# Kernel optimization log

Hardware: AMD Instinct MI355X
Metric: run time of the kernel (lower is better)

The kernel has to match this reference:

```python
import jax, jax.numpy as jnp
import numpy as np

H = W = 128
BS = 16
# Ragged per-canvas stroke counts (sum = 2048)
LENGTHS = np.array([64, 192, 128, 96, 160, 224, 32, 128, 128, 256, 64, 96, 160, 128, 96, 96], dtype=np.int64)
L = int(LENGTHS.sum())


def setup_inputs() -> dict:
    key = jax.random.key(0)
    k1, k2, k3 = jax.random.split(key, 3)
    u = jax.random.uniform(k1, (L, 8), dtype=jnp.float32)
    # keep stroke width/height in [0.1, 0.6] so 1/w, 1/h stay well-conditioned
    strokes = u.at[:, 2:4].set(0.1 + 0.5 * u[:, 2:4])
    meta_brushes = jax.random.uniform(k2, (2, 1, H, W), dtype=jnp.float32)
    start_canvas = jax.random.uniform(k3, (BS, 3, H, W), dtype=jnp.float32)
    return {"strokes": strokes, "meta_brushes": meta_brushes,
            "start_canvas": start_canvas, "lengths": LENGTHS}


def _grid_sample_bilinear(img, gx, gy):
    """torch.nn.functional.grid_sample(mode='bilinear', padding_mode='zeros',
    align_corners=False) for single-channel images.
    img: [L, H, W]; gx, gy: [L, Ho, Wo] normalized coords in [-1, 1]."""
    Lb, Hi, Wi = img.shape
    ix = (gx + 1.0) * (Wi * 0.5) - 0.5
    iy = (gy + 1.0) * (Hi * 0.5) - 0.5
    x0 = jnp.floor(ix)
    y0 = jnp.floor(iy)
    x1 = x0 + 1.0
    y1 = y0 + 1.0
    wx1 = ix - x0
    wx0 = 1.0 - wx1
    wy1 = iy - y0
    wy0 = 1.0 - wy1
    bidx = jnp.arange(Lb)[:, None, None]

    def tap(xf, yf):
        xi = jnp.clip(xf, 0, Wi - 1).astype(jnp.int32)
        yi = jnp.clip(yf, 0, Hi - 1).astype(jnp.int32)
        valid = (xf >= 0) & (xf <= Wi - 1) & (yf >= 0) & (yf <= Hi - 1)
        return jnp.where(valid, img[bidx, yi, xi], 0.0)

    return (wy0 * wx0 * tap(x0, y0) + wy0 * wx1 * tap(x1, y0)
            + wy1 * wx0 * tap(x0, y1) + wy1 * wx1 * tap(x1, y1))


def _strokes2brushes(strokes, meta_brushes):
    """Per-stroke affine warp of the meta brush (affine_grid + grid_sample)."""
    x0, y0, w, h, theta = [strokes[:, i] for i in range(5)]
    colors = strokes[:, 5:8]  # [L, 3]
    idx = (h <= w).astype(jnp.int32)          # vertical vs horizontal brush
    imgs = meta_brushes[idx, 0]               # [L, H, W]

    rad = theta * jnp.pi
    s, c = jnp.sin(rad), jnp.cos(rad)
    w00 = c / w
    w01 = s * H / (W * w)
    w02 = (1 - 2 * x0) * w00 + (1 - 2 * y0) * w01
    w10 = -s * W / (H * h)
    w11 = c / h
    w12 = (1 - 2 * y0) * w11 - (1 - 2 * x0) * (-w10)

    # affine_grid(align_corners=False): pixel-center normalized coords
    xs = (2.0 * jnp.arange(W) + 1.0) / W - 1.0  # [W]
    ys = (2.0 * jnp.arange(H) + 1.0) / H - 1.0  # [H]
    gxb, gyb = jnp.meshgrid(xs, ys)             # [H, W] each
    gx = w00[:, None, None] * gxb + w01[:, None, None] * gyb + w02[:, None, None]
    gy = w10[:, None, None] * gxb + w11[:, None, None] * gyb + w12[:, None, None]

    brushes = _grid_sample_bilinear(imgs, gx, gy)  # [L, H, W]
    return colors, brushes


def _forward(strokes, meta_brushes, start_canvas, lengths):
    lengths = np.asarray(lengths)
    bs = len(lengths)
    colors, brushes = _strokes2brushes(strokes, meta_brushes)
    alphas = jnp.where(brushes <= 0.6, brushes, 1.0)  # [L, H, W]

    # Segmented reverse-cumsum (flip->cumsum->flip minus self), vectorized:
    # suffix_excl_i = seg_total - inclusive_prefix_i
    ends = np.cumsum(lengths)                 # [bs]
    starts = ends - lengths                   # [bs]
    seg = np.repeat(np.arange(bs), lengths)   # [L] static segment ids
    csum = jnp.cumsum(alphas, axis=0)         # [L, H, W]
    csum_pad = jnp.concatenate([jnp.zeros((1, H, W), csum.dtype), csum], axis=0)
    pre = csum_pad[starts]                    # [bs, H, W] cumsum before seg start
    totals = csum_pad[ends] - pre             # [bs, H, W] per-segment alpha sum
    suffix_excl = totals[seg] - (csum - pre[seg])

    b = jnp.clip(brushes - suffix_excl, 0.0, 1.0)  # [L, H, W]
    canvas = jax.ops.segment_sum(colors[:, :, None, None] * b[:, None],
                                 seg, num_segments=bs)  # [bs, 3, H, W]
    canvas_alpha = jnp.clip(totals, 0.0, 1.0)           # [bs, H, W]

    # F.interpolate to (H, W) is identity here (start_canvas already HxW)
    canvas = canvas + start_canvas * (1.0 - canvas_alpha[:, None])
    return canvas.astype(jnp.float32)


def reference(strokes, meta_brushes, start_canvas, lengths):
    return _forward(strokes, meta_brushes, start_canvas, lengths)
```

## Files before the change

kernel.cpp:

```cpp
#include <hip/hip_runtime.h>

#define HW_ 16384
#define BS_ 16

static __device__ __constant__ int g_start[BS_] = {
    0, 64, 256, 384, 480, 640, 864, 896,
    1024, 1152, 1408, 1472, 1568, 1728, 1856, 1952};
static __device__ __constant__ int g_len[BS_] = {
    64, 192, 128, 96, 160, 224, 32, 128,
    128, 256, 64, 96, 160, 128, 96, 96};
static __device__ __constant__ int g_perm[BS_] = {
    9, 5, 1, 12, 4, 2, 7, 8, 0, 3, 11, 13, 6, 10, 14, 15};
static __device__ __constant__ int g_txor[4] = {0, 27, 45, 54};

__global__ __launch_bounds__(256) void light_render_kernel(
    const float* __restrict__ strokes,
    const float* __restrict__ meta,
    const float* __restrict__ start_canvas,
    float* __restrict__ out)
{
    __shared__ float sc[256 * 12];
    __shared__ unsigned short slist[4 * 256];
    __shared__ int s_wcnt[4];

    const int b    = g_perm[blockIdx.x >> 6];
    const int tile = (blockIdx.x & 63) ^ g_txor[blockIdx.x >> 8];
    const int tx = tile & 7, ty = tile >> 3;
    const int t    = threadIdx.x;
    const int lane = t & 63, wid = t >> 6;
    const int qx = wid & 1, qy = wid >> 1;
    const int c0p = (tx << 4) + (qx << 3);
    const int r0p = (ty << 4) + (qy << 3);
    const int col = c0p + (lane & 7);
    const int row = r0p + (lane >> 3);
    const int p   = (row << 7) + col;
    const int sg0 = g_start[b];
    const int len = g_len[b];

    const float cxb = (float)(32 * tx + 16) * 0.0078125f - 1.0f;
    const float cyb = (float)(32 * ty + 16) * 0.0078125f - 1.0f;
    const float exb = 15.0f / 128.0f;

    float d0=0,d1=0,d2=0,d3=0,d4=0,d5=0,d6=0,d7=0,d8=0,d9=0;
    bool keep = false;
    if (t < len) {
        const float4* sp = (const float4*)(strokes + (size_t)(sg0 + t) * 8);
        const float4 s0 = sp[0];
        const float4 s1 = sp[1];
        float sn, cs;
        sincosf(s1.x * 3.14159274101257324f, &sn, &cs);
        const float iw = 64.0f / s0.z;
        const float ih = 64.0f / s0.w;
        const float W00 = cs * iw, W01 = sn * iw;
        const float W10 = -sn * ih, W11 = cs * ih;
        const float ax = 1.0f - 2.0f * s0.x;
        const float ay = 1.0f - 2.0f * s0.y;
        const float W02 = fmaf(ax, W00, fmaf(ay, W01, 63.5f));
        const float W12 = fmaf(ay, W11, fmaf(ax, W10, 63.5f));
        const float cx = fmaf(W00, cxb, fmaf(W01, cyb, W02));
        const float cy = fmaf(W10, cxb, fmaf(W11, cyb, W12));
        const float rx = fabsf(W00) * exb + fabsf(W01) * exb;
        const float ry = fabsf(W10) * exb + fabsf(W11) * exb;
        keep = (fabsf(cx - 63.5f) <= 65.5f + rx) &&
               (fabsf(cy - 63.5f) <= 65.5f + ry);
        d0 = W00; d1 = W01; d2 = W02; d3 = W10; d4 = W11; d5 = W12;
        d6 = s1.y; d7 = s1.z; d8 = s1.w;
        d9 = (s0.w <= s0.z) ? 16384.0f : 0.0f;
    }
    const unsigned long long ball = __ballot(keep);
    const int pre = __popcll(ball & ((1ull << lane) - 1ull));
    if (lane == 0) s_wcnt[wid] = __popcll(ball);
    __syncthreads();
    int woff = 0;
    #pragma unroll
    for (int i = 0; i < 3; ++i) woff += (i < wid) ? s_wcnt[i] : 0;
    const int total = s_wcnt[0] + s_wcnt[1] + s_wcnt[2] + s_wcnt[3];
    if (keep) {
        float* dst = sc + (size_t)(woff + pre) * 12;
        dst[0]=d0; dst[1]=d1; dst[2]=d2;  dst[3]=d3; dst[4]=d4;  dst[5]=d5;
        dst[6]=d6; dst[7]=d7; dst[8]=d8;  dst[9]=d9; dst[10]=0.f; dst[11]=0.f;
    }
    __syncthreads();

    const float4* sv = (const float4*)sc;
    const float wcx = (float)(2 * c0p + 8) * 0.0078125f - 1.0f;
    const float wcy = (float)(2 * r0p + 8) * 0.0078125f - 1.0f;
    const float wex = 7.0f / 128.0f;
    unsigned short* wl = slist + (wid << 8);
    int wn = 0;
    for (int base = 0; base < total; base += 64) {
        const int k = base + lane;
        bool kp = false;
        if (k < total) {
            const float4 a0 = sv[k * 3];
            const float4 a1 = sv[k * 3 + 1];
            const float cx = fmaf(a0.x, wcx, fmaf(a0.y, wcy, a0.z));
            const float cy = fmaf(a0.w, wcx, fmaf(a1.x, wcy, a1.y));
            const float rx = fabsf(a0.x) * wex + fabsf(a0.y) * wex;
            const float ry = fabsf(a0.w) * wex + fabsf(a1.x) * wex;
            kp = (fabsf(cx - 63.5f) <= 65.5f + rx) &&
                 (fabsf(cy - 63.5f) <= 65.5f + ry);
        }
        const unsigned long long bl = __ballot(kp);
        if (kp) {
            const int pr = __popcll(bl & ((1ull << lane) - 1ull));
            wl[wn + pr] = (unsigned short)k;
        }
        wn += __popcll(bl);
    }

    const float gxb = (float)(2 * col + 1) * 0.0078125f - 1.0f;
    const float gyb = (float)(2 * row + 1) * 0.0078125f - 1.0f;

    float accR = 0.0f, accG = 0.0f, accB = 0.0f;
    float S = 0.0f;

    int j = wn - 1;
    float4 a0, a1, a2;
    if (j >= 0) {
        const int k = wl[j];
        a0 = sv[k*3]; a1 = sv[k*3+1]; a2 = sv[k*3+2];
    }
    while (j >= 0) {
        const int jn = j - 1;
        int kn = 0;
        if (jn >= 0) kn = wl[jn];
        const float4 c0 = a0, c1 = a1, c2 = a2;
        if (jn >= 0) {
            a0 = sv[kn*3]; a1 = sv[kn*3+1]; a2 = sv[kn*3+2];
        }

        const float ixf = fmaf(c0.x, gxb, fmaf(c0.y, gyb, c0.z));
        const float iyf = fmaf(c0.w, gxb, fmaf(c1.x, gyb, c1.y));
        const bool inside = (ixf > -1.0f) && (ixf < 128.0f) &&
                            (iyf > -1.0f) && (iyf < 128.0f);
        if (inside && (S < 1.0f)) {
            const float x0f = floorf(ixf), y0f = floorf(iyf);
            float wx1 = ixf - x0f, wy1 = iyf - y0f;
            float wx0 = 1.0f - wx1, wy0 = 1.0f - wy1;
            if (x0f < 0.0f)    wx0 = 0.0f;
            if (x0f > 126.0f)  wx1 = 0.0f;
            if (y0f < 0.0f)    wy0 = 0.0f;
            if (y0f > 126.0f)  wy1 = 0.0f;

            const int ix0 = (int)x0f, iy0 = (int)y0f;
            const int xi0 = max(ix0, 0), xi1 = min(ix0 + 1, 127);
            const int yi0 = max(iy0, 0), yi1 = min(iy0 + 1, 127);

            const float* img = meta + (int)c2.y;
            const int row0 = yi0 << 7, row1 = yi1 << 7;
            const float t00 = img[row0 + xi0];
            const float t01 = img[row0 + xi1];
            const float t10 = img[row1 + xi0];
            const float t11 = img[row1 + xi1];

            const float v = wy0 * fmaf(wx0, t00, wx1 * t01) +
                            wy1 * fmaf(wx0, t10, wx1 * t11);

            const float alpha = (v <= 0.6f) ? v : 1.0f;
            const float bb = fminf(fmaxf(v - S, 0.0f), 1.0f);
            accR = fmaf(c1.z, bb, accR);
            accG = fmaf(c1.w, bb, accG);
            accB = fmaf(c2.x, bb, accB);
            S += alpha;
        }
        if (__all(S >= 1.0f)) break;
        j = jn;
    }

    const float rem = 1.0f - fminf(S, 1.0f);
    const size_t base = ((size_t)b * 3) << 14;
    out[base + p]          = fmaf(start_canvas[base + p],          rem, accR);
    out[base + HW_ + p]    = fmaf(start_canvas[base + HW_ + p],    rem, accG);
    out[base + 2*HW_ + p]  = fmaf(start_canvas[base + 2*HW_ + p],  rem, accB);
}

extern "C" void kernel_launch(void* const* d_in, const int* in_sizes, int n_in,
                              void* d_out, int out_size, void* d_ws, size_t ws_size,
                              hipStream_t stream) {
    const float* strokes      = (const float*)d_in[0];
    const float* meta_brushes = (const float*)d_in[1];
    const float* start_canvas = (const float*)d_in[2];
    float* out = (float*)d_out;

    dim3 grid(BS_ * 64);
    dim3 block(256);
    light_render_kernel<<<grid, block, 0, stream>>>(strokes, meta_brushes,
                                                    start_canvas, out);
}
```

Before: 14.32 us.

## Software-pipeline brush texel gathers two strokes ahead in compositing loop

The per-pixel back-to-front compositing loop is restructured into a two-stage pipeline. Each stroke's bilinear weights and four meta-brush texel loads are issued one to two iterations before their values are blended, using two register slots (A/B) that alternate. The goal is to hide global-memory gather latency behind the blending arithmetic of the previous stroke. The cost is extra registers, some speculative loads for strokes that would have been skipped, and an early-exit check only every two strokes, with a simple scalar loop handling any leftover stroke.

```diff
diff --git a/kernel.cpp b/kernel.cpp
--- a/kernel.cpp
+++ b/kernel.cpp
@@ -12,6 +12,50 @@
 static __device__ __constant__ int g_perm[BS_] = {
     9, 5, 1, 12, 4, 2, 7, 8, 0, 3, 11, 13, 6, 10, 14, 15};
 static __device__ __constant__ int g_txor[4] = {0, 27, 45, 54};
+
+#define PREF(JJ, P)                                                          \
+  {                                                                          \
+    const int k_ = wl[JJ];                                                   \
+    const float4 c0_ = sv[k_ * 3];                                           \
+    const float4 c1_ = sv[k_ * 3 + 1];                                       \
+    const float4 c2_ = sv[k_ * 3 + 2];                                       \
+    const float ixf_ = fmaf(c0_.x, gxb, fmaf(c0_.y, gyb, c0_.z));            \
+    const float iyf_ = fmaf(c0_.w, gxb, fmaf(c1_.x, gyb, c1_.y));            \
+    const bool in_ = (ixf_ > -1.0f) && (ixf_ < 128.0f) &&                    \
+                     (iyf_ > -1.0f) && (iyf_ < 128.0f) && (S < 1.0f);        \
+    const float x0f_ = floorf(ixf_), y0f_ = floorf(iyf_);                    \
+    float wx1_ = ixf_ - x0f_, wy1_ = iyf_ - y0f_;                            \
+    float wx0_ = 1.0f - wx1_, wy0_ = 1.0f - wy1_;                            \
+    if (x0f_ < 0.0f)   wx0_ = 0.0f;                                          \
+    if (x0f_ > 126.0f) wx1_ = 0.0f;                                          \
+    if (y0f_ < 0.0f)   wy0_ = 0.0f;                                          \
+    if (y0f_ > 126.0f) wy1_ = 0.0f;                                          \
+    P##wx0 = wx0_; P##wx1 = wx1_; P##wy0 = wy0_; P##wy1 = wy1_;              \
+    P##cR = c1_.z; P##cG = c1_.w; P##cB = c2_.x;                             \
+    P##live = in_ ? 1.0f : 0.0f;                                             \
+    if (in_) {                                                               \
+      const int ix0_ = (int)x0f_, iy0_ = (int)y0f_;                          \
+      const int xi0_ = max(ix0_, 0), xi1_ = min(ix0_ + 1, 127);              \
+      const int yi0_ = max(iy0_, 0), yi1_ = min(iy0_ + 1, 127);              \
+      const float* img_ = meta + (int)c2_.y;                                 \
+      const int r0_ = yi0_ << 7, r1_ = yi1_ << 7;                            \
+      P##t00 = img_[r0_ + xi0_]; P##t01 = img_[r0_ + xi1_];                  \
+      P##t10 = img_[r1_ + xi0_]; P##t11 = img_[r1_ + xi1_];                  \
+    }                                                                        \
+  }
+
+#define COMP(P)                                                              \
+  {                                                                          \
+    const float v_ = P##live *                                               \
+        (P##wy0 * fmaf(P##wx0, P##t00, P##wx1 * P##t01) +                    \
+         P##wy1 * fmaf(P##wx0, P##t10, P##wx1 * P##t11));                    \
+    const float alpha_ = (v_ <= 0.6f) ? v_ : 1.0f;                           \
+    const float bb_ = fminf(fmaxf(v_ - S, 0.0f), 1.0f);                      \
+    accR = fmaf(P##cR, bb_, accR);                                           \
+    accG = fmaf(P##cG, bb_, accG);                                           \
+    accB = fmaf(P##cB, bb_, accB);                                           \
+    S += alpha_;                                                             \
+  }
 
 __global__ __launch_bounds__(256) void light_render_kernel(
     const float* __restrict__ strokes,
@@ -115,21 +159,32 @@
     float accR = 0.0f, accG = 0.0f, accB = 0.0f;
     float S = 0.0f;
 
+    float At00=0,At01=0,At10=0,At11=0,Awx0=0,Awx1=0,Awy0=0,Awy1=0,
+          Alive=0,AcR=0,AcG=0,AcB=0;
+    float Bt00=0,Bt01=0,Bt10=0,Bt11=0,Bwx0=0,Bwx1=0,Bwy0=0,Bwy1=0,
+          Blive=0,BcR=0,BcG=0,BcB=0;
+
     int j = wn - 1;
-    float4 a0, a1, a2;
-    if (j >= 0) {
+    if (j >= 3) {
+        PREF(j, A)
+        PREF(j - 1, B)
+        while (j >= 3) {
+            COMP(A)
+            PREF(j - 2, A)
+            COMP(B)
+            PREF(j - 3, B)
+            j -= 2;
+            if (__all(S >= 1.0f)) { j = -1; break; }
+        }
+        if (j >= 1) {
+            COMP(A)
+            COMP(B)
+            j -= 2;
+        }
+    }
+    while (j >= 0) {
         const int k = wl[j];
-        a0 = sv[k*3]; a1 = sv[k*3+1]; a2 = sv[k*3+2];
-    }
-    while (j >= 0) {
-        const int jn = j - 1;
-        int kn = 0;
-        if (jn >= 0) kn = wl[jn];
-        const float4 c0 = a0, c1 = a1, c2 = a2;
-        if (jn >= 0) {
-            a0 = sv[kn*3]; a1 = sv[kn*3+1]; a2 = sv[kn*3+2];
-        }
-
+        const float4 c0 = sv[k*3], c1 = sv[k*3+1], c2 = sv[k*3+2];
         const float ixf = fmaf(c0.x, gxb, fmaf(c0.y, gyb, c0.z));
         const float iyf = fmaf(c0.w, gxb, fmaf(c1.x, gyb, c1.y));
         const bool inside = (ixf > -1.0f) && (ixf < 128.0f) &&
@@ -142,21 +197,17 @@
             if (x0f > 126.0f)  wx1 = 0.0f;
             if (y0f < 0.0f)    wy0 = 0.0f;
             if (y0f > 126.0f)  wy1 = 0.0f;
-
             const int ix0 = (int)x0f, iy0 = (int)y0f;
             const int xi0 = max(ix0, 0), xi1 = min(ix0 + 1, 127);
             const int yi0 = max(iy0, 0), yi1 = min(iy0 + 1, 127);
-
             const float* img = meta + (int)c2.y;
-            const int row0 = yi0 << 7, row1 = yi1 << 7;
-            const float t00 = img[row0 + xi0];
-            const float t01 = img[row0 + xi1];
-            const float t10 = img[row1 + xi0];
-            const float t11 = img[row1 + xi1];
-
+            const int r0 = yi0 << 7, r1 = yi1 << 7;
+            const float t00 = img[r0 + xi0];
+            const float t01 = img[r0 + xi1];
+            const float t10 = img[r1 + xi0];
+            const float t11 = img[r1 + xi1];
             const float v = wy0 * fmaf(wx0, t00, wx1 * t01) +
                             wy1 * fmaf(wx0, t10, wx1 * t11);
-
             const float alpha = (v <= 0.6f) ? v : 1.0f;
             const float bb = fminf(fmaxf(v - S, 0.0f), 1.0f);
             accR = fmaf(c1.z, bb, accR);
@@ -164,8 +215,7 @@
             accB = fmaf(c2.x, bb, accB);
             S += alpha;
         }
-        if (__all(S >= 1.0f)) break;
-        j = jn;
+        --j;
     }
 
     const float rem = 1.0f - fminf(S, 1.0f);
```

Measured after the change: 14.02 us. 1.02x faster.
